# Optimization experiments

Hardware: AMD Instinct MI355X
Metric: run time of the kernel (lower is better)

## Reference

```python
import jax, jax.numpy as jnp
import numpy as np

IN_FEATURES = 512
OUT_FEATURES = 512
GRID_MIN = -2.0
GRID_MAX = 2.0
NUM_GRIDS = 8
SPLINE_SCALE = 0.1
BATCH = 16384


def setup_inputs() -> dict:
    key = jax.random.key(0)
    kx, kw = jax.random.split(key)
    x = jax.random.normal(kx, (BATCH, IN_FEATURES), dtype=jnp.float32)
    grid = jnp.linspace(GRID_MIN, GRID_MAX, NUM_GRIDS, dtype=jnp.float32)
    spline_weight = (
        jax.random.normal(kw, (IN_FEATURES * NUM_GRIDS, OUT_FEATURES), dtype=jnp.float32)
        * SPLINE_SCALE
    )
    return {"x": x, "grid": grid, "spline_weight": spline_weight}


def reference(x, grid, spline_weight):
    # denominator h = (grid_max - grid_min) / (num_grids - 1)
    h = (GRID_MAX - GRID_MIN) / (NUM_GRIDS - 1)
    # basis: [B, in_features, num_grids]
    basis = jnp.exp(-jnp.square((x[..., None] - grid) / h))
    # flatten to [B, in_features * num_grids] and GEMM
    return basis.reshape(basis.shape[0], -1) @ spline_weight
```

## Files before the change

kernel.cpp:

```cpp
#include <hip/hip_runtime.h>
#include <hip/hip_bf16.h>

#define BATCH 16384
#define IN_F 512
#define OUT_F 512
#define NG 8
#define KTOT (IN_F * NG)

#define SH    2.1019642153762872f
#define SSTEP 1.2011224087864498f
#define BC0N  4.2039284307525745f
#define RC1   2.4022448175728996f
#define RC2  -1.4426950408889634f
#define RQ    0.13533528323661270f

typedef __attribute__((ext_vector_type(8))) short short8;
typedef __attribute__((ext_vector_type(4))) float f32x4;
typedef __attribute__((ext_vector_type(2))) float f32x2;
typedef __attribute__((ext_vector_type(4))) unsigned int u32x4;
typedef __attribute__((ext_vector_type(2))) unsigned int u32x2;

__device__ __forceinline__ unsigned fbits(float f) {
    union { float f; unsigned u; } v; v.f = f; return v.u;
}
__device__ __forceinline__ unsigned pack2bf(float lo, float hi) {
    unsigned a = (fbits(lo) + 0x8000u) >> 16;
    unsigned b = (fbits(hi) + 0x8000u) & 0xFFFF0000u;
    return a | b;
}

__device__ __forceinline__ void lds_barrier() {
    __asm__ volatile("" ::: "memory");
    __builtin_amdgcn_sched_barrier(0);
    __builtin_amdgcn_s_waitcnt(0xC07F);
    __builtin_amdgcn_s_barrier();
    __builtin_amdgcn_sched_barrier(0);
    __asm__ volatile("" ::: "memory");
}

__global__ void wt_swizzle(const float* __restrict__ W, unsigned short* __restrict__ Wt) {
    const int gid  = blockIdx.x * 256 + threadIdx.x;
    const int lane = gid & 63;
    const int f    = (gid >> 6) & 7;
    const int kt   = (gid >> 9) & 63;
    const int s    = gid >> 15;
    const int j  = f & 3, kk = f >> 2;
    const int l15 = lane & 15, lq = lane >> 4;
    const int n  = s * 64 + j * 16 + l15;
    const int k0 = kt * 64 + kk * 32 + lq * 8;
    u32x4 pk;
#pragma unroll
    for (int e = 0; e < 4; ++e)
        pk[e] = pack2bf(W[(size_t)(k0 + 2 * e) * OUT_F + n],
                        W[(size_t)(k0 + 2 * e + 1) * OUT_F + n]);
    *(u32x4*)(Wt + (size_t)gid * 8) = pk;
}

__global__ __launch_bounds__(256, 2) void gauss_gemm5(
        const float* __restrict__ X, const unsigned short* __restrict__ Wt,
        float* __restrict__ Out) {
    __shared__ __align__(16) unsigned short sA[2 * 64 * 64];

    const int tid  = threadIdx.x;
    const int lane = tid & 63;
    const int wave = tid >> 6;
    const int cb = blockIdx.x & 1;
    const int rb = blockIdx.x >> 1;
    const int m0 = rb * 64;
    const int n0 = cb * 256;
    const int l15 = lane & 15;
    const int lq  = lane >> 4;
    const int s   = cb * 4 + wave;

    const int aw0 = lane * 64 + (((2 * wave)     ^ (lane & 7)) << 3);
    const int aw1 = lane * 64 + (((2 * wave + 1) ^ (lane & 7)) << 3);
    const float* xlp = X + (size_t)(m0 + lane) * IN_F + wave * 2;

    int aofs[2][4];
#pragma unroll
    for (int kk = 0; kk < 2; ++kk)
#pragma unroll
        for (int i = 0; i < 4; ++i)
            aofs[kk][i] = (i * 16 + l15) * 64 + (((kk * 4 + lq) ^ (l15 & 7)) << 3);

    const unsigned short* bptr = Wt + (size_t)s * 262144 + lane * 8;

    f32x4 acc[4][4];
#pragma unroll
    for (int i = 0; i < 4; ++i)
#pragma unroll
        for (int j = 0; j < 4; ++j)
            acc[i][j] = (f32x4){0.f, 0.f, 0.f, 0.f};

    auto stageA = [&](f32x2 xv, int buf) {
        unsigned short* base = sA + buf * 4096;
#pragma unroll
        for (int h = 0; h < 2; ++h) {
            const float t0 = fmaf(h ? xv.y : xv.x, SH, BC0N);
            float r = __builtin_amdgcn_exp2f(fmaf(t0, RC1, RC2));
            const float v0 = __builtin_amdgcn_exp2f(-t0 * t0);
            const float v1 = v0 * r;
            r *= RQ; const float v2 = v1 * r;
            r *= RQ; const float v3 = v2 * r;
            r *= RQ; const float v4 = v3 * r;
            r *= RQ; const float v5 = v4 * r;
            r *= RQ; const float v6 = v5 * r;
            r *= RQ; const float v7 = v6 * r;
            u32x4 pk;
            pk[0] = pack2bf(v0, v1);
            pk[1] = pack2bf(v2, v3);
            pk[2] = pack2bf(v4, v5);
            pk[3] = pack2bf(v6, v7);
            *(u32x4*)(base + (h ? aw1 : aw0)) = pk;
        }
    };

    short8 bfA[8], bfB[8];
    f32x2 xr;

    {
        f32x2 x0 = *(const f32x2*)(xlp);
        stageA(x0, 0);
#pragma unroll
        for (int f = 0; f < 8; ++f)
            bfA[f] = *(const short8*)(bptr + f * 512);
        xr = *(const f32x2*)(xlp + 8);
        lds_barrier();
    }

#define GG_ITER(KT, BUF, BU, BF)                                               \
    {                                                                          \
        const int kn1 = ((KT) + 1 < 63) ? (KT) + 1 : 63;                       \
        const int kn2 = ((KT) + 2 < 63) ? (KT) + 2 : 63;                       \
        short8 af[2][4];                                                       \
        _Pragma("unroll")                                                      \
        for (int kk = 0; kk < 2; ++kk)                                         \
            _Pragma("unroll")                                                  \
            for (int i = 0; i < 4; ++i)                                        \
                af[kk][i] = *(const short8*)(sA + (BUF) * 4096 + aofs[kk][i]); \
        _Pragma("unroll")                                                      \
        for (int f = 0; f < 8; ++f)                                            \
            BF[f] = *(const short8*)(bptr + (size_t)kn1 * 4096 + f * 512);     \
        stageA(xr, (BUF) ^ 1);                                                 \
        xr = *(const f32x2*)(xlp + (size_t)kn2 * 8);                           \
        _Pragma("unroll")                                                      \
        for (int kk = 0; kk < 2; ++kk)                                         \
            _Pragma("unroll")                                                  \
            for (int i = 0; i < 4; ++i)                                        \
                _Pragma("unroll")                                              \
                for (int j = 0; j < 4; ++j)                                    \
                    acc[i][j] = __builtin_amdgcn_mfma_f32_16x16x32_bf16(       \
                        af[kk][i], BU[kk * 4 + j], acc[i][j], 0, 0, 0);        \
        lds_barrier();                                                         \
    }

    for (int kt = 0; kt < 64; kt += 2) {
        GG_ITER(kt,     0, bfA, bfB)
        GG_ITER(kt + 1, 1, bfB, bfA)
    }
#undef GG_ITER

#pragma unroll
    for (int i = 0; i < 4; ++i) {
        const int r0 = m0 + i * 16 + lq * 4;
#pragma unroll
        for (int j = 0; j < 4; ++j) {
            const int c = n0 + wave * 64 + j * 16 + l15;
#pragma unroll
            for (int e = 0; e < 4; ++e)
                Out[(size_t)(r0 + e) * OUT_F + c] = acc[i][j][e];
        }
    }
}

#define BM 128
#define BN 128
#define BK 64
#define LDA 72
#define LDB 72

__global__ __launch_bounds__(256, 2) void gauss_gemm_fb(
        const float* __restrict__ X, const float* __restrict__ W,
        float* __restrict__ Out) {
    __shared__ __align__(16) unsigned short sA[BM * LDA];
    __shared__ __align__(16) unsigned short sB2[BN * LDB];

    const int tid  = threadIdx.x;
    const int lane = tid & 63;
    const int wave = tid >> 6;
    const int rb = blockIdx.x >> 2;
    const int cbx = blockIdx.x & 3;
    const int m0 = rb * BM;
    const int n0 = cbx * BN;
    const int wr = (wave >> 1) * 64;
    const int wc = (wave & 1) * 64;
    const int l15 = lane & 15;
    const int lq  = lane >> 4;

    f32x4 acc[4][4];
#pragma unroll
    for (int i = 0; i < 4; ++i)
#pragma unroll
        for (int j = 0; j < 4; ++j)
            acc[i][j] = (f32x4){0.f, 0.f, 0.f, 0.f};

    const int arow = tid & 127;
    const int axq  = tid >> 7;

    for (int kt = 0; kt < KTOT / BK; ++kt) {
        const int k0  = kt * BK;
        const int xc0 = kt * (BK / NG);

        const f32x4 xv = *(const f32x4*)(X + (size_t)(m0 + arow) * IN_F + xc0 + 4 * axq);
        unsigned short* sArow = sA + arow * LDA + axq * 32;
#pragma unroll
        for (int j = 0; j < 4; ++j) {
            const float xs = xv[j] * SH;
            u32x4 pk;
#pragma unroll
            for (int g = 0; g < 8; g += 2) {
                float t0 = xs + (BC0N - g * SSTEP);
                float t1 = xs + (BC0N - (g + 1) * SSTEP);
                unsigned u0 = fbits(__builtin_amdgcn_exp2f(-t0 * t0)) + 0x8000u;
                unsigned u1 = fbits(__builtin_amdgcn_exp2f(-t1 * t1)) + 0x8000u;
                pk[g >> 1] = (u0 >> 16) | (u1 & 0xFFFF0000u);
            }
            *(u32x4*)(sArow + j * 8) = pk;
        }

#pragma unroll
        for (int p = 0; p < 8; ++p) {
            int id = p * 256 + tid;
            int n  = id & 127;
            int k4 = id >> 7;
            const float* wp = W + (size_t)(k0 + k4 * 4) * OUT_F + n0 + n;
            u32x2 v;
            v[0] = pack2bf(wp[0], wp[OUT_F]);
            v[1] = pack2bf(wp[2 * OUT_F], wp[3 * OUT_F]);
            *(u32x2*)(sB2 + n * LDB + k4 * 4) = v;
        }

        __syncthreads();

#pragma unroll
        for (int kk = 0; kk < BK; kk += 32) {
            short8 af[4], bfv[4];
#pragma unroll
            for (int i = 0; i < 4; ++i)
                af[i] = *(const short8*)(sA + (wr + i * 16 + l15) * LDA + kk + lq * 8);
#pragma unroll
            for (int i = 0; i < 4; ++i)
                bfv[i] = *(const short8*)(sB2 + (wc + i * 16 + l15) * LDB + kk + lq * 8);
#pragma unroll
            for (int i = 0; i < 4; ++i)
#pragma unroll
                for (int j = 0; j < 4; ++j)
                    acc[i][j] = __builtin_amdgcn_mfma_f32_16x16x32_bf16(af[i], bfv[j], acc[i][j], 0, 0, 0);
        }

        __syncthreads();
    }

#pragma unroll
    for (int i = 0; i < 4; ++i) {
        const int r0 = m0 + wr + i * 16 + lq * 4;
#pragma unroll
        for (int j = 0; j < 4; ++j) {
            const int c = n0 + wc + j * 16 + l15;
#pragma unroll
            for (int e = 0; e < 4; ++e)
                Out[(size_t)(r0 + e) * OUT_F + c] = acc[i][j][e];
        }
    }
}

extern "C" void kernel_launch(void* const* d_in, const int* in_sizes, int n_in,
                              void* d_out, int out_size, void* d_ws, size_t ws_size,
                              hipStream_t stream) {
    (void)in_sizes; (void)n_in; (void)out_size;
    const float* X = (const float*)d_in[0];
    const float* W = (const float*)d_in[2];
    float* Out = (float*)d_out;

    const size_t wt_bytes = (size_t)KTOT * OUT_F * sizeof(unsigned short);
    if (ws_size >= wt_bytes) {
        unsigned short* Wt = (unsigned short*)d_ws;
        wt_swizzle<<<dim3(KTOT * OUT_F / 8 / 256), 256, 0, stream>>>(W, Wt);
        gauss_gemm5<<<dim3((BATCH / 64) * (OUT_F / 256)), 256, 0, stream>>>(X, Wt, Out);
    } else {
        gauss_gemm_fb<<<dim3((BATCH / BM) * (OUT_F / BN)), 256, 0, stream>>>(X, W, Out);
    }
}
```

Before: 153.7 us.

## Compute Gaussian basis directly in MFMA A-fragments, drop LDS staging

Each wave now builds its own A-operand fragments in registers from x, so the LDS double buffer and per-step barriers are gone. A constant per-grid factor of the Gaussian recurrence is folded into the pre-swizzled bf16 weights, which leaves the in-kernel recurrence as a plain multiply by one ratio. Wave priority is raised around the MFMA block. The cost is redundant work: every wave of both column blocks recomputes the same basis values, and tiny weight scale factors together with large unscaled basis terms could change bf16 rounding or push values out of range.

```diff
diff --git a/kernel.cpp b/kernel.cpp
--- a/kernel.cpp
+++ b/kernel.cpp
@@ -11,12 +11,9 @@
 #define SSTEP 1.2011224087864498f
 #define BC0N  4.2039284307525745f
 #define RC1   2.4022448175728996f
-#define RC2  -1.4426950408889634f
-#define RQ    0.13533528323661270f
 
 typedef __attribute__((ext_vector_type(8))) short short8;
 typedef __attribute__((ext_vector_type(4))) float f32x4;
-typedef __attribute__((ext_vector_type(2))) float f32x2;
 typedef __attribute__((ext_vector_type(4))) unsigned int u32x4;
 typedef __attribute__((ext_vector_type(2))) unsigned int u32x2;
 
@@ -24,18 +21,28 @@
     union { float f; unsigned u; } v; v.f = f; return v.u;
 }
 __device__ __forceinline__ unsigned pack2bf(float lo, float hi) {
-    unsigned a = (fbits(lo) + 0x8000u) >> 16;
-    unsigned b = (fbits(hi) + 0x8000u) & 0xFFFF0000u;
-    return a | b;
-}
-
-__device__ __forceinline__ void lds_barrier() {
-    __asm__ volatile("" ::: "memory");
-    __builtin_amdgcn_sched_barrier(0);
-    __builtin_amdgcn_s_waitcnt(0xC07F);
-    __builtin_amdgcn_s_barrier();
-    __builtin_amdgcn_sched_barrier(0);
-    __asm__ volatile("" ::: "memory");
+    return __builtin_amdgcn_perm(fbits(hi) + 0x8000u, fbits(lo) + 0x8000u,
+                                 0x07060302u);
+}
+
+__device__ __forceinline__ short8 basis_frag(float x) {
+    const float t0  = fmaf(x, SH, BC0N);
+    const float rho = __builtin_amdgcn_exp2f(t0 * RC1);
+    const float v0  = __builtin_amdgcn_exp2f(-t0 * t0);
+    const float v1 = v0 * rho;
+    const float v2 = v1 * rho;
+    const float v3 = v2 * rho;
+    const float v4 = v3 * rho;
+    const float v5 = v4 * rho;
+    const float v6 = v5 * rho;
+    const float v7 = v6 * rho;
+    u32x4 pk;
+    pk[0] = pack2bf(v0, v1);
+    pk[1] = pack2bf(v2, v3);
+    pk[2] = pack2bf(v4, v5);
+    pk[3] = pack2bf(v6, v7);
+    union { u32x4 u; short8 s; } cv; cv.u = pk;
+    return cv.s;
 }
 
 __global__ void wt_swizzle(const float* __restrict__ W, unsigned short* __restrict__ Wt) {
@@ -48,19 +55,25 @@
     const int l15 = lane & 15, lq = lane >> 4;
     const int n  = s * 64 + j * 16 + l15;
     const int k0 = kt * 64 + kk * 32 + lq * 8;
+    constexpr float QS[8] = {1.0f,
+                             3.6787944117144233e-1f,
+                             1.8315638888734179e-2f,
+                             1.2340980408667956e-4f,
+                             1.1253517471925912e-7f,
+                             1.3887943864964021e-11f,
+                             2.3195228302435693e-16f,
+                             5.2428856633634640e-22f};
     u32x4 pk;
 #pragma unroll
     for (int e = 0; e < 4; ++e)
-        pk[e] = pack2bf(W[(size_t)(k0 + 2 * e) * OUT_F + n],
-                        W[(size_t)(k0 + 2 * e + 1) * OUT_F + n]);
+        pk[e] = pack2bf(W[(size_t)(k0 + 2 * e) * OUT_F + n] * QS[2 * e],
+                        W[(size_t)(k0 + 2 * e + 1) * OUT_F + n] * QS[2 * e + 1]);
     *(u32x4*)(Wt + (size_t)gid * 8) = pk;
 }
 
-__global__ __launch_bounds__(256, 2) void gauss_gemm5(
+__global__ __launch_bounds__(256, 2) void gauss_gemm6(
         const float* __restrict__ X, const unsigned short* __restrict__ Wt,
         float* __restrict__ Out) {
-    __shared__ __align__(16) unsigned short sA[2 * 64 * 64];
-
     const int tid  = threadIdx.x;
     const int lane = tid & 63;
     const int wave = tid >> 6;
@@ -72,18 +85,12 @@
     const int lq  = lane >> 4;
     const int s   = cb * 4 + wave;
 
-    const int aw0 = lane * 64 + (((2 * wave)     ^ (lane & 7)) << 3);
-    const int aw1 = lane * 64 + (((2 * wave + 1) ^ (lane & 7)) << 3);
-    const float* xlp = X + (size_t)(m0 + lane) * IN_F + wave * 2;
-
-    int aofs[2][4];
-#pragma unroll
-    for (int kk = 0; kk < 2; ++kk)
-#pragma unroll
-        for (int i = 0; i < 4; ++i)
-            aofs[kk][i] = (i * 16 + l15) * 64 + (((kk * 4 + lq) ^ (l15 & 7)) << 3);
-
     const unsigned short* bptr = Wt + (size_t)s * 262144 + lane * 8;
+
+    const float* xrow[4];
+#pragma unroll
+    for (int i = 0; i < 4; ++i)
+        xrow[i] = X + (size_t)(m0 + i * 16 + l15) * IN_F + lq;
 
     f32x4 acc[4][4];
 #pragma unroll
@@ -92,57 +99,32 @@
         for (int j = 0; j < 4; ++j)
             acc[i][j] = (f32x4){0.f, 0.f, 0.f, 0.f};
 
-    auto stageA = [&](f32x2 xv, int buf) {
-        unsigned short* base = sA + buf * 4096;
-#pragma unroll
-        for (int h = 0; h < 2; ++h) {
-            const float t0 = fmaf(h ? xv.y : xv.x, SH, BC0N);
-            float r = __builtin_amdgcn_exp2f(fmaf(t0, RC1, RC2));
-            const float v0 = __builtin_amdgcn_exp2f(-t0 * t0);
-            const float v1 = v0 * r;
-            r *= RQ; const float v2 = v1 * r;
-            r *= RQ; const float v3 = v2 * r;
-            r *= RQ; const float v4 = v3 * r;
-            r *= RQ; const float v5 = v4 * r;
-            r *= RQ; const float v6 = v5 * r;
-            r *= RQ; const float v7 = v6 * r;
-            u32x4 pk;
-            pk[0] = pack2bf(v0, v1);
-            pk[1] = pack2bf(v2, v3);
-            pk[2] = pack2bf(v4, v5);
-            pk[3] = pack2bf(v6, v7);
-            *(u32x4*)(base + (h ? aw1 : aw0)) = pk;
-        }
-    };
-
     short8 bfA[8], bfB[8];
-    f32x2 xr;
-
-    {
-        f32x2 x0 = *(const f32x2*)(xlp);
-        stageA(x0, 0);
-#pragma unroll
-        for (int f = 0; f < 8; ++f)
-            bfA[f] = *(const short8*)(bptr + f * 512);
-        xr = *(const f32x2*)(xlp + 8);
-        lds_barrier();
-    }
-
-#define GG_ITER(KT, BUF, BU, BF)                                               \
+    float  xA[8], xB[8];
+
+#pragma unroll
+    for (int f = 0; f < 8; ++f)
+        xA[f] = xrow[f & 3][(f >> 2) * 4];
+#pragma unroll
+    for (int f = 0; f < 8; ++f)
+        bfA[f] = *(const short8*)(bptr + f * 512);
+
+#define GG_ITER(KT, BU, BF, XC, XN)                                            \
     {                                                                          \
         const int kn1 = ((KT) + 1 < 63) ? (KT) + 1 : 63;                       \
-        const int kn2 = ((KT) + 2 < 63) ? (KT) + 2 : 63;                       \
+        _Pragma("unroll")                                                      \
+        for (int f = 0; f < 8; ++f)                                            \
+            XN[f] = xrow[f & 3][(size_t)kn1 * 8 + (f >> 2) * 4];               \
+        _Pragma("unroll")                                                      \
+        for (int f = 0; f < 8; ++f)                                            \
+            BF[f] = *(const short8*)(bptr + (size_t)kn1 * 4096 + f * 512);     \
         short8 af[2][4];                                                       \
         _Pragma("unroll")                                                      \
         for (int kk = 0; kk < 2; ++kk)                                         \
             _Pragma("unroll")                                                  \
             for (int i = 0; i < 4; ++i)                                        \
-                af[kk][i] = *(const short8*)(sA + (BUF) * 4096 + aofs[kk][i]); \
-        _Pragma("unroll")                                                      \
-        for (int f = 0; f < 8; ++f)                                            \
-            BF[f] = *(const short8*)(bptr + (size_t)kn1 * 4096 + f * 512);     \
-        stageA(xr, (BUF) ^ 1);                                                 \
-        xr = *(const f32x2*)(xlp + (size_t)kn2 * 8);                           \
+                af[kk][i] = basis_frag(XC[kk * 4 + i]);                        \
+        __builtin_amdgcn_s_setprio(1);                                         \
         _Pragma("unroll")                                                      \
         for (int kk = 0; kk < 2; ++kk)                                         \
             _Pragma("unroll")                                                  \
@@ -151,12 +133,12 @@
                 for (int j = 0; j < 4; ++j)                                    \
                     acc[i][j] = __builtin_amdgcn_mfma_f32_16x16x32_bf16(       \
                         af[kk][i], BU[kk * 4 + j], acc[i][j], 0, 0, 0);        \
-        lds_barrier();                                                         \
+        __builtin_amdgcn_s_setprio(0);                                         \
     }
 
     for (int kt = 0; kt < 64; kt += 2) {
-        GG_ITER(kt,     0, bfA, bfB)
-        GG_ITER(kt + 1, 1, bfB, bfA)
+        GG_ITER(kt,     bfA, bfB, xA, xB)
+        GG_ITER(kt + 1, bfB, bfA, xB, xA)
     }
 #undef GG_ITER
 
@@ -221,9 +203,8 @@
             for (int g = 0; g < 8; g += 2) {
                 float t0 = xs + (BC0N - g * SSTEP);
                 float t1 = xs + (BC0N - (g + 1) * SSTEP);
-                unsigned u0 = fbits(__builtin_amdgcn_exp2f(-t0 * t0)) + 0x8000u;
-                unsigned u1 = fbits(__builtin_amdgcn_exp2f(-t1 * t1)) + 0x8000u;
-                pk[g >> 1] = (u0 >> 16) | (u1 & 0xFFFF0000u);
+                pk[g >> 1] = pack2bf(__builtin_amdgcn_exp2f(-t0 * t0),
+                                     __builtin_amdgcn_exp2f(-t1 * t1));
             }
             *(u32x4*)(sArow + j * 8) = pk;
         }
@@ -286,7 +267,7 @@
     if (ws_size >= wt_bytes) {
         unsigned short* Wt = (unsigned short*)d_ws;
         wt_swizzle<<<dim3(KTOT * OUT_F / 8 / 256), 256, 0, stream>>>(W, Wt);
-        gauss_gemm5<<<dim3((BATCH / 64) * (OUT_F / 256)), 256, 0, stream>>>(X, Wt, Out);
+        gauss_gemm6<<<dim3((BATCH / 64) * (OUT_F / 256)), 256, 0, stream>>>(X, Wt, Out);
     } else {
         gauss_gemm_fb<<<dim3((BATCH / BM) * (OUT_F / BN)), 256, 0, stream>>>(X, W, Out);
     }
```

Result: slower. 231.3 us (+50.4%).
